# Kernel tuning notes

Measured on AMD Instinct MI355X. Metric: run time of the kernel, lower is better.

Reference implementation:

```python
import jax, jax.numpy as jnp
import numpy as np

N_AGENTS = 32
N_HEADS = 8
HEAD_DIM = 32          # atten_dim // n_heads
HID = 256              # rnn_hidden_dim
ATT = 256              # atten_dim
N_ACT = 32
NEG = -1e9             # finite stand-in for -inf; exp underflows to 0 in softmax


def setup_inputs() -> dict:
    key = jax.random.key(0)
    ks = jax.random.split(key, 20)
    B, N, E = 4096, 64, 128
    w = lambda k, shape: (jax.random.normal(k, shape, jnp.float32) * 0.05)
    return {
        "inputs": jax.random.normal(ks[0], (B, N, E), jnp.float32),
        "hidden_state": jax.random.normal(ks[1], (B, N_AGENTS, HID), jnp.float32) * 0.1,
        "fc1_w": w(ks[2], (HID, E)), "fc1_b": jnp.zeros((HID,), jnp.float32),
        "q_w": w(ks[3], (ATT, HID)), "q_b": jnp.zeros((ATT,), jnp.float32),
        "k_w": w(ks[4], (ATT, HID)), "k_b": jnp.zeros((ATT,), jnp.float32),
        "v_w": w(ks[5], (ATT, HID)), "v_b": jnp.zeros((ATT,), jnp.float32),
        "w_ih": w(ks[6], (3 * HID, ATT)), "w_hh": w(ks[7], (3 * HID, HID)),
        "b_ih": jnp.zeros((3 * HID,), jnp.float32), "b_hh": jnp.zeros((3 * HID,), jnp.float32),
        "out_w": w(ks[8], (N_ACT, HID)), "out_b": jnp.zeros((N_ACT,), jnp.float32),
        "obs_mask": jax.random.randint(ks[9], (B, N, N), 0, 2).astype(bool),
        "scenario_mask": jax.random.randint(ks[10], (B, N_AGENTS), 0, 2).astype(bool),
    }


def reference(inputs, hidden_state, fc1_w, fc1_b, q_w, q_b, k_w, k_b, v_w, v_b,
              w_ih, w_hh, b_ih, b_hh, out_w, out_b, obs_mask, scenario_mask):
    B, N, _ = inputs.shape
    A, nh, e = N_AGENTS, N_HEADS, HEAD_DIM
    # fc1 + ReLU: [B, N, HID]
    x = jax.nn.relu(inputs @ fc1_w.T + fc1_b)
    # multi-head projections; queries only for the first A entities (agents)
    q = (x[:, :A] @ q_w.T + q_b).reshape(B, A, nh, e).transpose(0, 2, 1, 3)   # [B,nh,A,e]
    k = (x @ k_w.T + k_b).reshape(B, N, nh, e).transpose(0, 2, 3, 1)          # [B,nh,e,N]
    v = jax.nn.relu(x @ v_w.T + v_b).reshape(B, N, nh, e).transpose(0, 2, 1, 3)  # [B,nh,N,e]
    score = jnp.einsum('bhae,bhen->bhan', q, k) / np.float32(np.sqrt(e))      # [B,nh,A,N]
    m = obs_mask[:, :A, :][:, None, :, :]                                      # [B,1,A,N]
    score = jnp.where(m, NEG, score)
    w = jax.nn.softmax(score, axis=-1)
    # original: fully-masked rows give NaN then are zeroed; here zero all masked slots
    w = jnp.where(m, 0.0, w)
    att = jnp.einsum('bhan,bhne->bhae', w, v)                                  # [B,nh,A,e]
    att = att.transpose(0, 2, 1, 3).reshape(B * A, nh * e)                     # [B*A, ATT]
    # GRUCell step (PyTorch gate ordering: r, z, n)
    h0 = hidden_state.reshape(B * A, HID)
    gi = att @ w_ih.T + b_ih
    gh = h0 @ w_hh.T + b_hh
    ir, iz, in_ = jnp.split(gi, 3, axis=-1)
    hr, hz, hn = jnp.split(gh, 3, axis=-1)
    r = jax.nn.sigmoid(ir + hr)
    z = jax.nn.sigmoid(iz + hz)
    n = jnp.tanh(in_ + r * hn)
    h = (1.0 - z) * n + z * h0
    h = h.reshape(B, A, HID)
    am = scenario_mask[:, :, None]                                             # [B,A,1]
    h = jnp.where(am, 0.0, h)
    q_out = h @ out_w.T + out_b
    q_out = jnp.where(am, 0.0, q_out)
    return q_out, h
```

## Files before the change

### kernel.cpp

```cpp
#include <hip/hip_runtime.h>


using bfrag = __attribute__((ext_vector_type(8))) short;
using ffrag = __attribute__((ext_vector_type(4))) float;

#define MFMA(a,b,c) __builtin_amdgcn_mfma_f32_16x16x32_bf16((a),(b),(c),0,0,0)
#define SWZ(row,col,S,xm) ((row)*(S) + ((((col)&~7) ^ (((row)&(xm))<<3)) | ((col)&7)))

#define OFF_A2   0L
#define OFF_FC1  67108864L
#define OFF_QW   67141632L
#define OFF_KW   67207168L
#define OFF_VW   67272704L
#define OFF_W6   67338240L
#define OFF_OW   67731456L
#define OFF_FLAG 67739648L
#define WS_NEED_BYTES 135479552L

__device__ inline unsigned short f2bf(float x){
  union { float f; unsigned u; } v; v.f = x;
  unsigned r = v.u + 0x7fffu + ((v.u >> 16) & 1u);
  return (unsigned short)(r >> 16);
}
__device__ inline float bf2f(short b){
  union { unsigned u; float f; } v; v.u = ((unsigned)(unsigned short)b) << 16;
  return v.f;
}
__device__ inline bool getmask(const void* p, long i, int byteflag){
  return byteflag ? (((const unsigned char*)p)[i] != 0)
                  : (((const int*)p)[i] != 0);
}
__device__ inline ffrag fzero(){ ffrag z; z[0]=0.f; z[1]=0.f; z[2]=0.f; z[3]=0.f; return z; }
__device__ inline void gload16(const short* g, short* l){
  __builtin_amdgcn_global_load_lds((const __attribute__((address_space(1))) void*)g,
                                   (__attribute__((address_space(3))) void*)l, 16, 0, 0);
}

__global__ void k0_prep(const float* __restrict__ fc1, const float* __restrict__ qw,
    const float* __restrict__ kw, const float* __restrict__ vw, const float* __restrict__ wih,
    const float* __restrict__ whh, const float* __restrict__ ow, const float* __restrict__ h0,
    const void* __restrict__ obsm, short* __restrict__ ws){
  long tid = (long)blockIdx.x*blockDim.x + threadIdx.x;
  long n = (long)gridDim.x*blockDim.x;
  if (tid == 0){
    const int* mi = (const int*)obsm;
    int f = 0;
    for (int i=0;i<256;i++){ if ((unsigned)mi[i] > 1u){ f = 1; break; } }
    ((int*)(ws + OFF_FLAG))[0] = f;
  }
  for (long i=tid; i<32768; i+=n) ws[OFF_FC1+i] = (short)f2bf(fc1[i]);
  for (long i=tid; i<65536; i+=n){
    ws[OFF_QW+i] = (short)f2bf(qw[i]);
    ws[OFF_KW+i] = (short)f2bf(kw[i]);
    ws[OFF_VW+i] = (short)f2bf(vw[i]);
  }
  for (long i=tid; i<196608; i+=n){
    int gate = (int)(i >> 16);
    int grow = (int)((i >> 8) & 255);
    int c = (int)(i & 255);
    int jb = grow >> 5, row = grow & 31;
    int cs = c ^ ((row&7)<<3);
    ws[OFF_W6 + ((long)((jb*6 + gate)*32 + row))*256 + cs]     = (short)f2bf(wih[i]);
    ws[OFF_W6 + ((long)((jb*6 + 3 + gate)*32 + row))*256 + cs] = (short)f2bf(whh[i]);
  }
  for (long i=tid; i<8192; i+=n) ws[OFF_OW+i] = (short)f2bf(ow[i]);
  const float2* h2 = (const float2*)h0;
  unsigned* a2u = (unsigned*)(ws + OFF_A2);
  for (long i=tid; i<16777216L; i+=n){
    long row = i >> 7; int j = (int)(i & 127);
    float2 v = h2[i];
    unsigned pk = (unsigned)f2bf(v.x) | ((unsigned)f2bf(v.y) << 16);
    a2u[row*256 + 128 + j] = pk;
  }
}

__global__ __launch_bounds__(512) void k1_fqkv(const float* __restrict__ inp,
    const short* __restrict__ fc1B, const float* __restrict__ fc1_b,
    const short* __restrict__ wq, const short* __restrict__ wk, const short* __restrict__ wv,
    const float* __restrict__ qb, const float* __restrict__ kb, const float* __restrict__ vb,
    short* __restrict__ A2, short* __restrict__ kC, short* __restrict__ vC, int chunkB){
  __shared__ __align__(16) short smem[65536];
  short* a_s  = smem;
  short* fw_s = smem + 16384;
  short* x_s  = smem;
  int t = threadIdx.x;
  long R0 = (long)blockIdx.x * 128;
  long grow0 = (long)chunkB*131072 + R0;
  int lane = t&63, w = t>>6, lr = lane&15, ko = lane>>4;
  for (int i=0;i<4;i++){
    int c = t + i*512; int row = c>>4; int cc = (c&15)*8;
    const float* src = inp + (grow0 + row)*128 + cc;
    float4 f0 = *(const float4*)src; float4 f1 = *(const float4*)(src+4);
    bfrag v8;
    v8[0]=(short)f2bf(f0.x); v8[1]=(short)f2bf(f0.y); v8[2]=(short)f2bf(f0.z); v8[3]=(short)f2bf(f0.w);
    v8[4]=(short)f2bf(f1.x); v8[5]=(short)f2bf(f1.y); v8[6]=(short)f2bf(f1.z); v8[7]=(short)f2bf(f1.w);
    *(bfrag*)(a_s + SWZ(row, cc, 128, 7)) = v8;
  }
  for (int i=0;i<8;i++){
    int c = t + i*512; int row = c>>4; int cc = (c&15)*8;
    *(bfrag*)(fw_s + SWZ(row, cc, 128, 7)) = *(const bfrag*)(fc1B + row*128 + cc);
  }
  __syncthreads();
  ffrag acc1[16];
  #pragma unroll
  for (int i=0;i<16;i++) acc1[i]=fzero();
  for (int ks=0; ks<4; ks++){
    int kc = ks*32 + ko*8;
    bfrag a = *(const bfrag*)(a_s + SWZ(w*16+lr, kc, 128, 7));
    #pragma unroll
    for (int nt=0; nt<16; nt++){
      bfrag bb = *(const bfrag*)(fw_s + SWZ(nt*16+lr, kc, 128, 7));
      acc1[nt] = MFMA(a, bb, acc1[nt]);
    }
  }
  __syncthreads();
  #pragma unroll
  for (int nt=0; nt<16; nt++){
    float bias = fc1_b[nt*16+lr];
    #pragma unroll
    for (int r=0;r<4;r++){
      int row = w*16 + ko*4 + r;
      float v = acc1[nt][r] + bias; v = v>0.f?v:0.f;
      x_s[SWZ(row, nt*16+lr, 256, 7)] = (short)f2bf(v);
    }
  }
  bfrag a_r[8];
  #pragma unroll
  for (int ks=0; ks<8; ks++)
    a_r[ks] = *(const bfrag*)(x_s + SWZ(w*16+lr, ks*32+ko*8, 256, 7));
  auto STAGE2 = [&](int s){
    int kind = s>>2; int rb = (s&3)*64;
    const short* wsrc = (kind==0?wq:(kind==1?wk:wv)) + (long)rb*256;
    short* dst = smem + 32768 + (s&1)*16384;
    #pragma unroll
    for (int i=0;i<4;i++){
      int c = t + i*512; int row = c>>5; int cc = (c&31)*8;
      *(bfrag*)(dst + SWZ(row, cc, 256, 7)) = *(const bfrag*)(wsrc + (long)row*256 + cc);
    }
  };
  STAGE2(0);
  __syncthreads();
  for (int s=0; s<12; s++){
    if (s < 11) STAGE2(s+1);
    const short* wcur = smem + 32768 + (s&1)*16384;
    ffrag acc2[4];
    #pragma unroll
    for (int i=0;i<4;i++) acc2[i]=fzero();
    #pragma unroll
    for (int ks=0; ks<8; ks++){
      int kc = ks*32 + ko*8;
      #pragma unroll
      for (int nt=0; nt<4; nt++){
        bfrag bb = *(const bfrag*)(wcur + SWZ(nt*16+lr, kc, 256, 7));
        acc2[nt] = MFMA(a_r[ks], bb, acc2[nt]);
      }
    }
    int kind = s>>2; int rb = (s&3)*64;
    const float* bsrc = (kind==0?qb:(kind==1?kb:vb));
    #pragma unroll
    for (int nt=0; nt<4; nt++){
      int colk = rb + nt*16 + lr;
      float bias = bsrc[colk];
      #pragma unroll
      for (int r=0;r<4;r++){
        int row = w*16 + ko*4 + r;
        long rl = R0 + row;
        float v = acc2[nt][r] + bias;
        if (kind==0){
          if ((row&32)==0){
            long grow = grow0 + row;
            long qrow = ((grow>>6)<<5) + (grow&31);
            A2[qrow*512 + colk] = (short)f2bf(v);
          }
        } else if (kind==1){
          kC[rl*256 + colk] = (short)f2bf(v);
        } else {
          v = v>0.f?v:0.f;
          vC[rl*256 + colk] = (short)f2bf(v);
        }
      }
    }
    __syncthreads();
  }
}

__global__ __launch_bounds__(512,4) void k2_attn(const short* __restrict__ kC,
    const short* __restrict__ vC, const void* __restrict__ obsm, short* __restrict__ A2,
    const int* __restrict__ flagp, int chunkB){
  __shared__ __align__(16) short vT_s[8][2048];
  __shared__ __align__(16) short p_s[8][2048];
  __shared__ unsigned char m_s[2048];
  int t = threadIdx.x, bl = blockIdx.x;
  long b = (long)chunkB*2048 + bl;
  int lane = t&63, w = t>>6, lr = lane&15, ko = lane>>4;
  int mflag = *flagp;
  if (mflag){
    uchar4 mv = *(const uchar4*)((const unsigned char*)obsm + b*4096 + t*4);
    m_s[t*4]=mv.x; m_s[t*4+1]=mv.y; m_s[t*4+2]=mv.z; m_s[t*4+3]=mv.w;
  } else {
    int4 mv = *(const int4*)((const int*)obsm + b*4096 + t*4);
    m_s[t*4]  =(unsigned char)(mv.x!=0); m_s[t*4+1]=(unsigned char)(mv.y!=0);
    m_s[t*4+2]=(unsigned char)(mv.z!=0); m_s[t*4+3]=(unsigned char)(mv.w!=0);
  }
  const int h = w;
  const short* qh = A2 + ((long)b*32)*512 + h*32 + ko*8;
  bfrag a_q[2];
  #pragma unroll
  for (int mt=0; mt<2; mt++) a_q[mt] = *(const bfrag*)(qh + (long)(mt*16+lr)*512);
  const short* kh = kC + ((long)bl*64)*256 + h*32 + ko*8;
  bfrag b_k[4];
  #pragma unroll
  for (int nt=0; nt<4; nt++) b_k[nt] = *(const bfrag*)(kh + (nt*16+lr)*256);
  #pragma unroll
  for (int i=0;i<4;i++){
    int n = i*16 + (lane>>2); int e0 = (lane&3)*8;
    bfrag vv = *(const bfrag*)(vC + ((long)bl*64 + n)*256 + h*32 + e0);
    #pragma unroll
    for (int j=0;j<8;j++) vT_s[w][SWZ(e0+j, n, 64, 7)] = vv[j];
  }
  ffrag sc[2][4];
  #pragma unroll
  for (int mt=0; mt<2; mt++)
    #pragma unroll
    for (int nt=0; nt<4; nt++) sc[mt][nt] = MFMA(a_q[mt], b_k[nt], fzero());
  __syncthreads();
  const float scale = 0.17677669529663687f;
  float rsi[2][4];
  #pragma unroll
  for (int mt=0; mt<2; mt++){
    #pragma unroll
    for (int r=0; r<4; r++){
      int arow = mt*16 + ko*4 + r;
      float sv[4]; int mk[4];
      #pragma unroll
      for (int nt=0; nt<4; nt++){
        mk[nt] = m_s[arow*64 + nt*16 + lr];
        sv[nt] = sc[mt][nt][r] * scale;
      }
      float mx = -3.0e38f;
      #pragma unroll
      for (int nt=0; nt<4; nt++) if (!mk[nt]) mx = fmaxf(mx, sv[nt]);
      for (int d=1; d<16; d<<=1) mx = fmaxf(mx, __shfl_xor(mx, d));
      float sum = 0.f;
      #pragma unroll
      for (int nt=0; nt<4; nt++){
        float p = mk[nt] ? 0.f : __expf(sv[nt]-mx);
        sv[nt] = p; sum += p;
      }
      for (int d=1; d<16; d<<=1) sum += __shfl_xor(sum, d);
      rsi[mt][r] = sum > 0.f ? 1.f/sum : 0.f;
      #pragma unroll
      for (int nt=0; nt<4; nt++)
        p_s[w][SWZ(arow, nt*16+lr, 64, 7)] = (short)f2bf(sv[nt]);
    }
  }
  ffrag o[2][2];
  #pragma unroll
  for (int mt=0;mt<2;mt++)
    #pragma unroll
    for (int nt=0;nt<2;nt++) o[mt][nt]=fzero();
  #pragma unroll
  for (int kk=0; kk<2; kk++){
    int kc = kk*32 + ko*8;
    bfrag pa0 = *(const bfrag*)(p_s[w]  + SWZ(lr,    kc, 64, 7));
    bfrag pa1 = *(const bfrag*)(p_s[w]  + SWZ(16+lr, kc, 64, 7));
    bfrag bv0 = *(const bfrag*)(vT_s[w] + SWZ(lr,    kc, 64, 7));
    bfrag bv1 = *(const bfrag*)(vT_s[w] + SWZ(16+lr, kc, 64, 7));
    o[0][0]=MFMA(pa0,bv0,o[0][0]); o[0][1]=MFMA(pa0,bv1,o[0][1]);
    o[1][0]=MFMA(pa1,bv0,o[1][0]); o[1][1]=MFMA(pa1,bv1,o[1][1]);
  }
  #pragma unroll
  for (int mt=0; mt<2; mt++)
    #pragma unroll
    for (int nt=0; nt<2; nt++)
      #pragma unroll
      for (int r=0; r<4; r++){
        int a = mt*16 + ko*4 + r;
        A2[((long)b*32 + a)*512 + h*32 + nt*16 + lr] = (short)f2bf(o[mt][nt][r]*rsi[mt][r]);
      }
}

__global__ __launch_bounds__(512) void k3_gru(const short* __restrict__ A2,
    const short* __restrict__ w6, const float* __restrict__ b_ih, const float* __restrict__ b_hh,
    const void* __restrict__ scen, float* __restrict__ hout, const int* __restrict__ flagp){
  __shared__ __align__(16) short w_s[2][16384];
  int t = threadIdx.x, bid = blockIdx.x;
  long R0 = (long)bid * 128;
  int mflag = *flagp;
  int lane = t&63, w = t>>6, lr = lane&15, ko = lane>>4;
  long rowbase = R0 + (long)w*16;
  auto STAGE = [&](int ph){
    const short* src = w6 + (long)ph*16384;
    short* dst = w_s[ph&1];
    #pragma unroll
    for (int i=0;i<4;i++)
      gload16(src + (long)(i*512 + t)*8, dst + (i*512 + (t & ~63))*8);
  };
  STAGE(0);
  const short* Ab = A2 + (rowbase + lr)*512 + ko*8;
  bfrag A[16];
  #pragma unroll
  for (int ks=0; ks<16; ks++)
    A[ks] = *(const bfrag*)(Ab + ks*32);
  __syncthreads();
  for (int jb=0; jb<8; jb++){
    ffrag aR[2], aZ[2], aI[2], aN[2];
    #pragma unroll
    for (int nt=0;nt<2;nt++){ aR[nt]=fzero(); aZ[nt]=fzero(); aI[nt]=fzero(); aN[nt]=fzero(); }
    #pragma unroll
    for (int p=0; p<3; p++){
      int ph = jb*3 + p;
      if (ph < 23) STAGE(ph+1);
      const short* wc = w_s[ph&1];
      #pragma unroll
      for (int ks=0; ks<8; ks++){
        int kc = ks*32 + ko*8;
        #pragma unroll
        for (int nt=0; nt<2; nt++){
          bfrag b0 = *(const bfrag*)(wc + SWZ(nt*16+lr, kc, 256, 7));
          bfrag b1 = *(const bfrag*)(wc + 8192 + SWZ(nt*16+lr, kc, 256, 7));
          if (p == 0){
            aR[nt] = MFMA(A[ks], b0, aR[nt]);
            aZ[nt] = MFMA(A[ks], b1, aZ[nt]);
          } else if (p == 1){
            aI[nt] = MFMA(A[ks], b0, aI[nt]);
            aR[nt] = MFMA(A[8+ks], b1, aR[nt]);
          } else {
            aZ[nt] = MFMA(A[8+ks], b0, aZ[nt]);
            aN[nt] = MFMA(A[8+ks], b1, aN[nt]);
          }
        }
      }
      if (p == 2){
        #pragma unroll
        for (int nt=0; nt<2; nt++){
          int j = jb*32 + nt*16 + lr;
          float bir = b_ih[j],     bhr = b_hh[j];
          float biz = b_ih[256+j], bhz = b_hh[256+j];
          float bin = b_ih[512+j], bhn = b_hh[512+j];
          #pragma unroll
          for (int rr=0; rr<4; rr++){
            long row = rowbase + ko*4 + rr;
            float rg = 1.f/(1.f + __expf(-(aR[nt][rr] + bir + bhr)));
            float zg = 1.f/(1.f + __expf(-(aZ[nt][rr] + biz + bhz)));
            float ag = aI[nt][rr] + bin + rg*(aN[nt][rr] + bhn);
            float ng = 2.f/(1.f + __expf(-2.f*ag)) - 1.f;
            float h0v = bf2f(A2[row*512 + 256 + j]);
            float hv = (1.f - zg)*ng + zg*h0v;
            if (getmask(scen, row, mflag)) hv = 0.f;
            hout[row*256 + j] = hv;
          }
        }
      }
      __syncthreads();
    }
  }
}

__global__ __launch_bounds__(512) void k4_out(const float* __restrict__ hout,
    const short* __restrict__ ow, const float* __restrict__ out_b,
    const void* __restrict__ scen, float* __restrict__ qout, const int* __restrict__ flagp){
  __shared__ __align__(16) short ow_s[32*256];
  int t = threadIdx.x; long R0 = (long)blockIdx.x * 256;
  int mflag = *flagp;
  for (int i=0;i<2;i++){
    int c = t + i*512; int row = c >> 5; int cc = (c & 31)*8;
    *(bfrag*)(ow_s + SWZ(row, cc, 256, 7)) = *(const bfrag*)(ow + row*256 + cc);
  }
  __syncthreads();
  int lane = t&63, w = t>>6, lr = lane&15, ko = lane>>4;
  ffrag acc[2][2];
  #pragma unroll
  for (int a=0;a<2;a++) for (int bq=0;bq<2;bq++) acc[a][bq]=fzero();
  for (int ks=0; ks<8; ks++){
    int kc = ks*32 + ko*8;
    #pragma unroll
    for (int mi=0; mi<2; mi++){
      long row = R0 + (w*2+mi)*16 + lr;
      const float* hp = hout + row*256 + kc;
      float4 f0 = *(const float4*)hp; float4 f1 = *(const float4*)(hp+4);
      bfrag a;
      a[0]=(short)f2bf(f0.x); a[1]=(short)f2bf(f0.y); a[2]=(short)f2bf(f0.z); a[3]=(short)f2bf(f0.w);
      a[4]=(short)f2bf(f1.x); a[5]=(short)f2bf(f1.y); a[6]=(short)f2bf(f1.z); a[7]=(short)f2bf(f1.w);
      #pragma unroll
      for (int nt=0; nt<2; nt++){
        bfrag bb = *(const bfrag*)(ow_s + SWZ(nt*16+lr, kc, 256, 7));
        acc[mi][nt] = MFMA(a, bb, acc[mi][nt]);
      }
    }
  }
  #pragma unroll
  for (int mi=0;mi<2;mi++)
    #pragma unroll
    for (int nt=0;nt<2;nt++){
      int col = nt*16 + lr;
      float ob = out_b[col];
      #pragma unroll
      for (int r=0;r<4;r++){
        long row = R0 + (w*2+mi)*16 + ko*4 + r;
        float qv = acc[mi][nt][r] + ob;
        if (getmask(scen, row, mflag)) qv = 0.f;
        qout[row*32 + col] = qv;
      }
    }
}

extern "C" void kernel_launch(void* const* d_in, const int* in_sizes, int n_in,
                              void* d_out, int out_size, void* d_ws, size_t ws_size,
                              hipStream_t stream){
  const float* inputs = (const float*)d_in[0];
  const float* hidden = (const float*)d_in[1];
  const float* fc1_w  = (const float*)d_in[2];
  const float* fc1_b  = (const float*)d_in[3];
  const float* q_w    = (const float*)d_in[4];
  const float* q_b    = (const float*)d_in[5];
  const float* k_w    = (const float*)d_in[6];
  const float* k_b    = (const float*)d_in[7];
  const float* v_w    = (const float*)d_in[8];
  const float* v_b    = (const float*)d_in[9];
  const float* w_ih   = (const float*)d_in[10];
  const float* w_hh   = (const float*)d_in[11];
  const float* b_ih   = (const float*)d_in[12];
  const float* b_hh   = (const float*)d_in[13];
  const float* out_w  = (const float*)d_in[14];
  const float* out_b  = (const float*)d_in[15];
  const void* obsm    = d_in[16];
  const void* scen    = d_in[17];
  (void)in_sizes; (void)n_in; (void)out_size;
  if ((long)ws_size < WS_NEED_BYTES) return;
  short* ws = (short*)d_ws;
  const int* flagp = (const int*)(ws + OFF_FLAG);
  float* qout = (float*)d_out;
  float* hout = qout + 4194304;
  short* kCs = (short*)hout;
  short* vCs = kCs + 33554432L;
  short* A2  = ws + OFF_A2;

  hipLaunchKernelGGL(k0_prep, dim3(2048), dim3(256), 0, stream,
      fc1_w, q_w, k_w, v_w, w_ih, w_hh, out_w, hidden, obsm, ws);
  for (int c=0; c<2; c++){
    hipLaunchKernelGGL(k1_fqkv, dim3(1024), dim3(512), 0, stream,
        inputs, ws + OFF_FC1, fc1_b, ws + OFF_QW, ws + OFF_KW, ws + OFF_VW,
        q_b, k_b, v_b, A2, kCs, vCs, c);
    hipLaunchKernelGGL(k2_attn, dim3(2048), dim3(512), 0, stream,
        kCs, vCs, obsm, A2, flagp, c);
  }
  hipLaunchKernelGGL(k3_gru, dim3(1024), dim3(512), 0, stream,
      A2, ws + OFF_W6, b_ih, b_hh, scen, hout, flagp);
  hipLaunchKernelGGL(k4_out, dim3(512), dim3(512), 0, stream,
      hout, ws + OFF_OW, out_b, scen, qout, flagp);
}
```

Before: 612.5 us.

## Drop bf16 hidden-state staging; GRU reads fp32 h0 directly, retile QKV projection

Removes the prep pass that converted the 128MB fp32 hidden state into a bf16 half of the A2 workspace. The GRU kernel now loads and packs h0 from fp32 directly, and A2 shrinks to a 256-wide row stride. Separately, the QKV projection in k1 is retiled so each wave computes 32 rows by 2 column tiles, which reuses each B fragment across two MFMAs. The cost is twice the register footprint for the A fragments, plus an extra sync. The GRU epilogue reads h0 in fp32, which also slightly changes numerics.

```diff
diff --git a/kernel.cpp b/kernel.cpp
--- a/kernel.cpp
+++ b/kernel.cpp
@@ -22,10 +22,6 @@
   unsigned r = v.u + 0x7fffu + ((v.u >> 16) & 1u);
   return (unsigned short)(r >> 16);
 }
-__device__ inline float bf2f(short b){
-  union { unsigned u; float f; } v; v.u = ((unsigned)(unsigned short)b) << 16;
-  return v.f;
-}
 __device__ inline bool getmask(const void* p, long i, int byteflag){
   return byteflag ? (((const unsigned char*)p)[i] != 0)
                   : (((const int*)p)[i] != 0);
@@ -35,10 +31,17 @@
   __builtin_amdgcn_global_load_lds((const __attribute__((address_space(1))) void*)g,
                                    (__attribute__((address_space(3))) void*)l, 16, 0, 0);
 }
+__device__ inline bfrag packbf(const float* p){
+  float4 f0 = *(const float4*)p; float4 f1 = *(const float4*)(p+4);
+  bfrag v;
+  v[0]=(short)f2bf(f0.x); v[1]=(short)f2bf(f0.y); v[2]=(short)f2bf(f0.z); v[3]=(short)f2bf(f0.w);
+  v[4]=(short)f2bf(f1.x); v[5]=(short)f2bf(f1.y); v[6]=(short)f2bf(f1.z); v[7]=(short)f2bf(f1.w);
+  return v;
+}
 
 __global__ void k0_prep(const float* __restrict__ fc1, const float* __restrict__ qw,
     const float* __restrict__ kw, const float* __restrict__ vw, const float* __restrict__ wih,
-    const float* __restrict__ whh, const float* __restrict__ ow, const float* __restrict__ h0,
+    const float* __restrict__ whh, const float* __restrict__ ow,
     const void* __restrict__ obsm, short* __restrict__ ws){
   long tid = (long)blockIdx.x*blockDim.x + threadIdx.x;
   long n = (long)gridDim.x*blockDim.x;
@@ -64,14 +67,6 @@
     ws[OFF_W6 + ((long)((jb*6 + 3 + gate)*32 + row))*256 + cs] = (short)f2bf(whh[i]);
   }
   for (long i=tid; i<8192; i+=n) ws[OFF_OW+i] = (short)f2bf(ow[i]);
-  const float2* h2 = (const float2*)h0;
-  unsigned* a2u = (unsigned*)(ws + OFF_A2);
-  for (long i=tid; i<16777216L; i+=n){
-    long row = i >> 7; int j = (int)(i & 127);
-    float2 v = h2[i];
-    unsigned pk = (unsigned)f2bf(v.x) | ((unsigned)f2bf(v.y) << 16);
-    a2u[row*256 + 128 + j] = pk;
-  }
 }
 
 __global__ __launch_bounds__(512) void k1_fqkv(const float* __restrict__ inp,
@@ -89,12 +84,7 @@
   int lane = t&63, w = t>>6, lr = lane&15, ko = lane>>4;
   for (int i=0;i<4;i++){
     int c = t + i*512; int row = c>>4; int cc = (c&15)*8;
-    const float* src = inp + (grow0 + row)*128 + cc;
-    float4 f0 = *(const float4*)src; float4 f1 = *(const float4*)(src+4);
-    bfrag v8;
-    v8[0]=(short)f2bf(f0.x); v8[1]=(short)f2bf(f0.y); v8[2]=(short)f2bf(f0.z); v8[3]=(short)f2bf(f0.w);
-    v8[4]=(short)f2bf(f1.x); v8[5]=(short)f2bf(f1.y); v8[6]=(short)f2bf(f1.z); v8[7]=(short)f2bf(f1.w);
-    *(bfrag*)(a_s + SWZ(row, cc, 128, 7)) = v8;
+    *(bfrag*)(a_s + SWZ(row, cc, 128, 7)) = packbf(inp + (grow0 + row)*128 + cc);
   }
   for (int i=0;i<8;i++){
     int c = t + i*512; int row = c>>4; int cc = (c&15)*8;
@@ -124,10 +114,14 @@
       x_s[SWZ(row, nt*16+lr, 256, 7)] = (short)f2bf(v);
     }
   }
-  bfrag a_r[8];
-  #pragma unroll
-  for (int ks=0; ks<8; ks++)
-    a_r[ks] = *(const bfrag*)(x_s + SWZ(w*16+lr, ks*32+ko*8, 256, 7));
+  __syncthreads();
+  int rg = w & 3, chs = w >> 2;
+  bfrag a_r[2][8];
+  #pragma unroll
+  for (int mt=0; mt<2; mt++)
+    #pragma unroll
+    for (int ks=0; ks<8; ks++)
+      a_r[mt][ks] = *(const bfrag*)(x_s + SWZ(rg*32+mt*16+lr, ks*32+ko*8, 256, 7));
   auto STAGE2 = [&](int s){
     int kind = s>>2; int rb = (s&3)*64;
     const short* wsrc = (kind==0?wq:(kind==1?wk:wv)) + (long)rb*256;
@@ -143,43 +137,47 @@
   for (int s=0; s<12; s++){
     if (s < 11) STAGE2(s+1);
     const short* wcur = smem + 32768 + (s&1)*16384;
-    ffrag acc2[4];
-    #pragma unroll
-    for (int i=0;i<4;i++) acc2[i]=fzero();
+    ffrag acc2[2][2];
+    #pragma unroll
+    for (int a=0;a<2;a++) for (int bq=0;bq<2;bq++) acc2[a][bq]=fzero();
     #pragma unroll
     for (int ks=0; ks<8; ks++){
       int kc = ks*32 + ko*8;
       #pragma unroll
-      for (int nt=0; nt<4; nt++){
-        bfrag bb = *(const bfrag*)(wcur + SWZ(nt*16+lr, kc, 256, 7));
-        acc2[nt] = MFMA(a_r[ks], bb, acc2[nt]);
+      for (int ntl=0; ntl<2; ntl++){
+        int ntc = chs*2 + ntl;
+        bfrag bb = *(const bfrag*)(wcur + SWZ(ntc*16+lr, kc, 256, 7));
+        acc2[0][ntl] = MFMA(a_r[0][ks], bb, acc2[0][ntl]);
+        acc2[1][ntl] = MFMA(a_r[1][ks], bb, acc2[1][ntl]);
       }
     }
     int kind = s>>2; int rb = (s&3)*64;
     const float* bsrc = (kind==0?qb:(kind==1?kb:vb));
     #pragma unroll
-    for (int nt=0; nt<4; nt++){
-      int colk = rb + nt*16 + lr;
-      float bias = bsrc[colk];
-      #pragma unroll
-      for (int r=0;r<4;r++){
-        int row = w*16 + ko*4 + r;
-        long rl = R0 + row;
-        float v = acc2[nt][r] + bias;
-        if (kind==0){
-          if ((row&32)==0){
-            long grow = grow0 + row;
-            long qrow = ((grow>>6)<<5) + (grow&31);
-            A2[qrow*512 + colk] = (short)f2bf(v);
+    for (int mt=0; mt<2; mt++)
+      #pragma unroll
+      for (int ntl=0; ntl<2; ntl++){
+        int colk = rb + (chs*2+ntl)*16 + lr;
+        float bias = bsrc[colk];
+        #pragma unroll
+        for (int r=0;r<4;r++){
+          int row = rg*32 + mt*16 + ko*4 + r;
+          long rl = R0 + row;
+          float v = acc2[mt][ntl][r] + bias;
+          if (kind==0){
+            if ((row&32)==0){
+              long grow = grow0 + row;
+              long qrow = ((grow>>6)<<5) + (grow&31);
+              A2[qrow*256 + colk] = (short)f2bf(v);
+            }
+          } else if (kind==1){
+            kC[rl*256 + colk] = (short)f2bf(v);
+          } else {
+            v = v>0.f?v:0.f;
+            vC[rl*256 + colk] = (short)f2bf(v);
           }
-        } else if (kind==1){
-          kC[rl*256 + colk] = (short)f2bf(v);
-        } else {
-          v = v>0.f?v:0.f;
-          vC[rl*256 + colk] = (short)f2bf(v);
         }
       }
-    }
     __syncthreads();
   }
 }
@@ -203,10 +201,10 @@
     m_s[t*4+2]=(unsigned char)(mv.z!=0); m_s[t*4+3]=(unsigned char)(mv.w!=0);
   }
   const int h = w;
-  const short* qh = A2 + ((long)b*32)*512 + h*32 + ko*8;
+  const short* qh = A2 + ((long)b*32)*256 + h*32 + ko*8;
   bfrag a_q[2];
   #pragma unroll
-  for (int mt=0; mt<2; mt++) a_q[mt] = *(const bfrag*)(qh + (long)(mt*16+lr)*512);
+  for (int mt=0; mt<2; mt++) a_q[mt] = *(const bfrag*)(qh + (long)(mt*16+lr)*256);
   const short* kh = kC + ((long)bl*64)*256 + h*32 + ko*8;
   bfrag b_k[4];
   #pragma unroll
@@ -276,12 +274,13 @@
       #pragma unroll
       for (int r=0; r<4; r++){
         int a = mt*16 + ko*4 + r;
-        A2[((long)b*32 + a)*512 + h*32 + nt*16 + lr] = (short)f2bf(o[mt][nt][r]*rsi[mt][r]);
+        A2[((long)b*32 + a)*256 + h*32 + nt*16 + lr] = (short)f2bf(o[mt][nt][r]*rsi[mt][r]);
       }
 }
 
 __global__ __launch_bounds__(512) void k3_gru(const short* __restrict__ A2,
-    const short* __restrict__ w6, const float* __restrict__ b_ih, const float* __restrict__ b_hh,
+    const float* __restrict__ h0f, const short* __restrict__ w6,
+    const float* __restrict__ b_ih, const float* __restrict__ b_hh,
     const void* __restrict__ scen, float* __restrict__ hout, const int* __restrict__ flagp){
   __shared__ __align__(16) short w_s[2][16384];
   int t = threadIdx.x, bid = blockIdx.x;
@@ -297,11 +296,15 @@
       gload16(src + (long)(i*512 + t)*8, dst + (i*512 + (t & ~63))*8);
   };
   STAGE(0);
-  const short* Ab = A2 + (rowbase + lr)*512 + ko*8;
+  const short* Ab = A2 + (rowbase + lr)*256 + ko*8;
+  const float* Hb = h0f + (rowbase + lr)*256 + ko*8;
   bfrag A[16];
   #pragma unroll
-  for (int ks=0; ks<16; ks++)
+  for (int ks=0; ks<8; ks++)
     A[ks] = *(const bfrag*)(Ab + ks*32);
+  #pragma unroll
+  for (int ks=0; ks<8; ks++)
+    A[8+ks] = packbf(Hb + ks*32);
   __syncthreads();
   for (int jb=0; jb<8; jb++){
     ffrag aR[2], aZ[2], aI[2], aN[2];
@@ -345,7 +348,7 @@
             float zg = 1.f/(1.f + __expf(-(aZ[nt][rr] + biz + bhz)));
             float ag = aI[nt][rr] + bin + rg*(aN[nt][rr] + bhn);
             float ng = 2.f/(1.f + __expf(-2.f*ag)) - 1.f;
-            float h0v = bf2f(A2[row*512 + 256 + j]);
+            float h0v = h0f[row*256 + j];
             float hv = (1.f - zg)*ng + zg*h0v;
             if (getmask(scen, row, mflag)) hv = 0.f;
             hout[row*256 + j] = hv;
@@ -377,11 +380,7 @@
     #pragma unroll
     for (int mi=0; mi<2; mi++){
       long row = R0 + (w*2+mi)*16 + lr;
-      const float* hp = hout + row*256 + kc;
-      float4 f0 = *(const float4*)hp; float4 f1 = *(const float4*)(hp+4);
-      bfrag a;
-      a[0]=(short)f2bf(f0.x); a[1]=(short)f2bf(f0.y); a[2]=(short)f2bf(f0.z); a[3]=(short)f2bf(f0.w);
-      a[4]=(short)f2bf(f1.x); a[5]=(short)f2bf(f1.y); a[6]=(short)f2bf(f1.z); a[7]=(short)f2bf(f1.w);
+      bfrag a = packbf(hout + row*256 + kc);
       #pragma unroll
       for (int nt=0; nt<2; nt++){
         bfrag bb = *(const bfrag*)(ow_s + SWZ(nt*16+lr, kc, 256, 7));
@@ -436,8 +435,8 @@
   short* vCs = kCs + 33554432L;
   short* A2  = ws + OFF_A2;
 
-  hipLaunchKernelGGL(k0_prep, dim3(2048), dim3(256), 0, stream,
-      fc1_w, q_w, k_w, v_w, w_ih, w_hh, out_w, hidden, obsm, ws);
+  hipLaunchKernelGGL(k0_prep, dim3(512), dim3(256), 0, stream,
+      fc1_w, q_w, k_w, v_w, w_ih, w_hh, out_w, obsm, ws);
   for (int c=0; c<2; c++){
     hipLaunchKernelGGL(k1_fqkv, dim3(1024), dim3(512), 0, stream,
         inputs, ws + OFF_FC1, fc1_b, ws + OFF_QW, ws + OFF_KW, ws + OFF_VW,
@@ -446,7 +445,7 @@
         kCs, vCs, obsm, A2, flagp, c);
   }
   hipLaunchKernelGGL(k3_gru, dim3(1024), dim3(512), 0, stream,
-      A2, ws + OFF_W6, b_ih, b_hh, scen, hout, flagp);
+      A2, hidden, ws + OFF_W6, b_ih, b_hh, scen, hout, flagp);
   hipLaunchKernelGGL(k4_out, dim3(512), dim3(512), 0, stream,
       hout, ws + OFF_OW, out_b, scen, qout, flagp);
 }
```

Result: no change. 614.3 us (+0.3%).
